# Optimization experiments

Measured on AMD Instinct MI355X. Metric: run time of the kernel, lower is better.

The kernel has to match this reference:

```python
import jax, jax.numpy as jnp
import numpy as np

DIM = 256
NUM_HEADS = 4
WINDOW = 64
EPS = 1e-6


def setup_inputs() -> dict:
    key = jax.random.key(0)
    ks = jax.random.split(key, 12)
    d = DIM
    s = 0.02
    return {
        "x": jax.random.normal(ks[0], (4, 2049, d), dtype=jnp.float32),
        "norm1_w": jnp.ones((d,), jnp.float32),
        "in_proj_w": jax.random.normal(ks[1], (3 * d, d), jnp.float32) * s,
        "in_proj_b": jnp.zeros((3 * d,), jnp.float32),
        "out_proj_w": jax.random.normal(ks[2], (d, d), jnp.float32) * s,
        "out_proj_b": jnp.zeros((d,), jnp.float32),
        "norm2_w": jnp.ones((d,), jnp.float32),
        "w1": jax.random.normal(ks[3], (2 * d, d), jnp.float32) * s,
        "b1": jnp.zeros((2 * d,), jnp.float32),
        "w2": jax.random.normal(ks[4], (d, 2 * d), jnp.float32) * s,
        "b2": jnp.zeros((d,), jnp.float32),
    }


def _rmsnorm(x, w):
    r = jax.lax.rsqrt(jnp.mean(x * x, axis=-1, keepdims=True) + EPS)
    return x * r * w


def _factorized_mask(size):
    # global token 0 attends/attended everywhere; others banded within WINDOW
    idx = jnp.arange(size)
    band = jnp.abs(idx[:, None] - idx[None, :]) <= WINDOW
    allowed = band | (idx[:, None] == 0) | (idx[None, :] == 0)
    return jnp.where(allowed, 0.0, -jnp.inf).astype(jnp.float32)


def reference(x, norm1_w, in_proj_w, in_proj_b, out_proj_w, out_proj_b,
              norm2_w, w1, b1, w2, b2):
    B, S, D = x.shape
    H = NUM_HEADS
    dh = D // H
    residual = x
    h = _rmsnorm(x, norm1_w)
    # fused qkv projection (torch MHA in_proj): [B,S,3D]
    qkv = h @ in_proj_w.T + in_proj_b
    q, k, v = jnp.split(qkv, 3, axis=-1)
    q = q.reshape(B, S, H, dh).transpose(0, 2, 1, 3)  # [B,H,S,dh]
    k = k.reshape(B, S, H, dh).transpose(0, 2, 1, 3)
    v = v.reshape(B, S, H, dh).transpose(0, 2, 1, 3)
    scores = jnp.einsum("bhqd,bhkd->bhqk", q, k) / jnp.sqrt(jnp.float32(dh))
    scores = scores + _factorized_mask(S)  # additive -inf mask
    attn = jax.nn.softmax(scores, axis=-1)
    ctx = jnp.einsum("bhqk,bhkd->bhqd", attn, v)
    ctx = ctx.transpose(0, 2, 1, 3).reshape(B, S, D)
    attn_out = ctx @ out_proj_w.T + out_proj_b
    x1 = residual + attn_out
    h2 = _rmsnorm(x1, norm2_w)
    ffn = jax.nn.gelu(h2 @ w1.T + b1, approximate=False) @ w2.T + b2
    return x1 + ffn
```

## Files before the change

### kernel.cpp

```cpp
#include <hip/hip_runtime.h>
#include <hip/hip_bf16.h>
#include <math.h>

#define BATCH 4
#define SEQ 2049
#define DIMD 256
#define WIN 64
#define M_ROWS (BATCH * SEQ)
#define M_PAD 8320

#define QT16 129
#define NKB 10
#define PSTR 168
#define CSTR 264
#define VGUARD 64
#define VW 2256
#define QKSTR 512

#define NSPLIT 33
#define VT_F4 288768

typedef __attribute__((ext_vector_type(8))) short short8;
typedef __attribute__((ext_vector_type(4))) float f32x4;
typedef __hip_bfloat16 bf16;

__device__ __forceinline__ float b2f(short u) {
    union { unsigned int i; float f; } c;
    c.i = ((unsigned int)(unsigned short)u) << 16;
    return c.f;
}
__device__ __forceinline__ short f2b(float f) {
    bf16 h = __float2bfloat16(f);
    return *reinterpret_cast<short*>(&h);
}

__global__ __launch_bounds__(256) void prep_kernel(
        const float* __restrict__ wq, const float* __restrict__ wo,
        const float* __restrict__ w1, const float* __restrict__ w2,
        bf16* __restrict__ oq, bf16* __restrict__ oo,
        bf16* __restrict__ o1, bf16* __restrict__ o2,
        const float* __restrict__ x, const float* __restrict__ nw,
        bf16* __restrict__ h, float4* __restrict__ vTz) {
    const int bi = blockIdx.x, tid = threadIdx.x;
    if (bi < 2048) {
        int i = bi * 256 + tid;
        if (i < 196608)      oq[i]          = __float2bfloat16(wq[i]);
        else if (i < 262144) oo[i - 196608] = __float2bfloat16(wo[i - 196608]);
        else if (i < 393216) o1[i - 262144] = __float2bfloat16(w1[i - 262144]);
        else                 o2[i - 393216] = __float2bfloat16(w2[i - 393216]);
        return;
    }
    if (bi >= 4097) {
        int zi = (bi - 4097) * 256 + tid;
        #pragma unroll
        for (int it = 0; it < 3; it++) {
            int idx = zi + it * 512 * 256;
            if (idx < VT_F4) vTz[idx] = (float4){0.f, 0.f, 0.f, 0.f};
        }
        return;
    }
    int wid = tid >> 6, lane = tid & 63;
    int row = (bi - 2048) * 4 + wid;
    if (row >= M_ROWS) return;
    const float4 v = reinterpret_cast<const float4*>(x + (size_t)row * DIMD)[lane];
    float ss = v.x * v.x + v.y * v.y + v.z * v.z + v.w * v.w;
    #pragma unroll
    for (int o = 1; o < 64; o <<= 1) ss += __shfl_xor(ss, o, 64);
    float r = rsqrtf(ss * (1.0f / DIMD) + 1e-6f);
    const float4 wv = reinterpret_cast<const float4*>(nw)[lane];
    bf16* hp = h + (size_t)row * DIMD + lane * 4;
    hp[0] = __float2bfloat16(v.x * r * wv.x);
    hp[1] = __float2bfloat16(v.y * r * wv.y);
    hp[2] = __float2bfloat16(v.z * r * wv.z);
    hp[3] = __float2bfloat16(v.w * r * wv.w);
}

__global__ __launch_bounds__(256) void gemm_qkv(
        const bf16* __restrict__ A, const bf16* __restrict__ B,
        const float* __restrict__ bias, bf16* __restrict__ qk, short* __restrict__ vT) {
    __shared__ __align__(16) short lA[8 * 64 * 8];
    __shared__ __align__(16) short lB[8 * 128 * 8];
    const int tid = threadIdx.x, lane = tid & 63, wid = tid >> 6;
    const int m0 = blockIdx.x * 64;
    const int n0 = blockIdx.y * 128;
    const int wr = wid >> 1, wc = wid & 1;
    const int r = lane & 15, g = lane >> 4;
    const int K = 256;

    f32x4 acc[2][4];
    #pragma unroll
    for (int i = 0; i < 2; i++)
        #pragma unroll
        for (int j = 0; j < 4; j++) acc[i][j] = (f32x4){0.f, 0.f, 0.f, 0.f};

    for (int k0 = 0; k0 < K; k0 += 64) {
        #pragma unroll
        for (int it = 0; it < 2; ++it) {
            int c = it * 256 + tid;
            int kc = c >> 6, row = c & 63;
            __builtin_amdgcn_global_load_lds(
                (const __attribute__((address_space(1))) void*)(A + (size_t)(m0 + row) * K + k0 + kc * 8),
                (__attribute__((address_space(3))) void*)&lA[c * 8], 16, 0, 0);
        }
        #pragma unroll
        for (int it = 0; it < 4; ++it) {
            int c = it * 256 + tid;
            int kc = c >> 7, row = c & 127;
            __builtin_amdgcn_global_load_lds(
                (const __attribute__((address_space(1))) void*)(B + (size_t)(n0 + row) * K + k0 + kc * 8),
                (__attribute__((address_space(3))) void*)&lB[c * 8], 16, 0, 0);
        }
        __syncthreads();
        #pragma unroll
        for (int kk = 0; kk < 2; kk++) {
            short8 a[2], b[4];
            #pragma unroll
            for (int mi = 0; mi < 2; mi++)
                a[mi] = *reinterpret_cast<const short8*>(&lA[((kk * 4 + g) * 64 + wr * 32 + mi * 16 + r) * 8]);
            #pragma unroll
            for (int ni = 0; ni < 4; ni++)
                b[ni] = *reinterpret_cast<const short8*>(&lB[((kk * 4 + g) * 128 + wc * 64 + ni * 16 + r) * 8]);
            #pragma unroll
            for (int mi = 0; mi < 2; mi++)
                #pragma unroll
                for (int ni = 0; ni < 4; ni++)
                    acc[mi][ni] = __builtin_amdgcn_mfma_f32_16x16x32_bf16(a[mi], b[ni], acc[mi][ni], 0, 0, 0);
        }
        __syncthreads();
    }

    const int c0 = lane & 15, r0 = (lane >> 4) * 4;
    const bool isV = (n0 >= 512);
    #pragma unroll
    for (int mi = 0; mi < 2; mi++) {
        #pragma unroll
        for (int ni = 0; ni < 4; ni++) {
            int col = n0 + wc * 64 + ni * 16 + c0;
            float bv = bias[col];
            #pragma unroll
            for (int j = 0; j < 4; j++) {
                int row = m0 + wr * 32 + mi * 16 + r0 + j;
                if (row < M_ROWS) {
                    float v = acc[mi][ni][j] + bv;
                    if (!isV) {
                        qk[(size_t)row * QKSTR + col] = __float2bfloat16(v);
                    } else {
                        int dcol = col - 512, hh = dcol >> 6, d = dcol & 63;
                        int bb = row >> 11;
                        int js = row - bb * SEQ;
                        if (js < 0) { bb--; js += SEQ; }
                        vT[((size_t)((bb * 4 + hh) * 64 + d)) * VW + VGUARD + js] = f2b(v);
                    }
                }
            }
        }
    }
}

template<int MODE, int BM, int BN>
__global__ __launch_bounds__(256) void gemm_lds(
        const bf16* __restrict__ A, const bf16* __restrict__ B,
        const float* __restrict__ bias, const float* __restrict__ resid,
        void* __restrict__ C, int M, int N, int K) {
    constexpr int FM = BM / 32;
    constexpr int FN = BN / 32;
    __shared__ __align__(16) short lA[8 * BM * 8];
    __shared__ __align__(16) short lB[8 * BN * 8];
    const int tid = threadIdx.x, lane = tid & 63, wid = tid >> 6;
    const int m0 = blockIdx.x * BM;
    const int n0 = blockIdx.y * BN;
    const int wr = wid >> 1, wc = wid & 1;
    const int r = lane & 15, g = lane >> 4;

    f32x4 acc[FM][FN];
    #pragma unroll
    for (int i = 0; i < FM; i++)
        #pragma unroll
        for (int j = 0; j < FN; j++) acc[i][j] = (f32x4){0.f, 0.f, 0.f, 0.f};

    for (int k0 = 0; k0 < K; k0 += 64) {
        #pragma unroll
        for (int it = 0; it < BM / 32; ++it) {
            int c = it * 256 + tid;
            int kc = c / BM, row = c % BM;
            __builtin_amdgcn_global_load_lds(
                (const __attribute__((address_space(1))) void*)(A + (size_t)(m0 + row) * K + k0 + kc * 8),
                (__attribute__((address_space(3))) void*)&lA[c * 8], 16, 0, 0);
        }
        #pragma unroll
        for (int it = 0; it < BN / 32; ++it) {
            int c = it * 256 + tid;
            int kc = c / BN, row = c % BN;
            __builtin_amdgcn_global_load_lds(
                (const __attribute__((address_space(1))) void*)(B + (size_t)(n0 + row) * K + k0 + kc * 8),
                (__attribute__((address_space(3))) void*)&lB[c * 8], 16, 0, 0);
        }
        __syncthreads();
        #pragma unroll
        for (int kk = 0; kk < 2; kk++) {
            short8 a[FM], b[FN];
            #pragma unroll
            for (int mi = 0; mi < FM; mi++)
                a[mi] = *reinterpret_cast<const short8*>(&lA[((kk * 4 + g) * BM + wr * (BM / 2) + mi * 16 + r) * 8]);
            #pragma unroll
            for (int ni = 0; ni < FN; ni++)
                b[ni] = *reinterpret_cast<const short8*>(&lB[((kk * 4 + g) * BN + wc * (BN / 2) + ni * 16 + r) * 8]);
            #pragma unroll
            for (int mi = 0; mi < FM; mi++)
                #pragma unroll
                for (int ni = 0; ni < FN; ni++)
                    acc[mi][ni] = __builtin_amdgcn_mfma_f32_16x16x32_bf16(a[mi], b[ni], acc[mi][ni], 0, 0, 0);
        }
        __syncthreads();
    }

    const int c0 = lane & 15, r0 = (lane >> 4) * 4;
    #pragma unroll
    for (int mi = 0; mi < FM; mi++) {
        #pragma unroll
        for (int ni = 0; ni < FN; ni++) {
            int col = n0 + wc * (BN / 2) + ni * 16 + c0;
            float bv = bias[col];
            #pragma unroll
            for (int j = 0; j < 4; j++) {
                int row = m0 + wr * (BM / 2) + mi * 16 + r0 + j;
                if (row < M) {
                    float v = acc[mi][ni][j] + bv;
                    if (MODE == 2) v = 0.5f * v * (1.0f + erff(v * 0.70710678118654752f));
                    if (MODE == 1) {
                        v += resid[(size_t)row * N + col];
                        reinterpret_cast<float*>(C)[(size_t)row * N + col] = v;
                    } else {
                        reinterpret_cast<bf16*>(C)[(size_t)row * N + col] = __float2bfloat16(v);
                    }
                }
            }
        }
    }
}

__global__ __launch_bounds__(256) void attn_partial(const bf16* __restrict__ qk,
                                                    const short* __restrict__ vT,
                                                    float* __restrict__ part) {
    __shared__ float q_s[64];
    __shared__ float p_s[64];
    __shared__ float meta[2];
    __shared__ float osum[4][64];
    const int tid = threadIdx.x;
    const int bh = blockIdx.x / NSPLIT, s = blockIdx.x % NSPLIT;
    const int b = bh >> 2, h = bh & 3;
    const size_t base = (size_t)b * SEQ;
    const int j0 = s * 64;
    const int lane = tid & 63, wid = tid >> 6;

    if (tid < 64) q_s[tid] = __bfloat162float(qk[base * QKSTR + h * 64 + tid]);
    __syncthreads();

    if (wid == 0) {
        int j = j0 + lane;
        float sc = -1e30f;
        if (j < SEQ) {
            const short8* kp = reinterpret_cast<const short8*>(
                reinterpret_cast<const short*>(qk) + (base + j) * QKSTR + 256 + h * 64);
            float acc = 0.f;
            #pragma unroll
            for (int d8 = 0; d8 < 8; ++d8) {
                short8 kv = kp[d8];
                #pragma unroll
                for (int e = 0; e < 8; ++e) acc += q_s[d8 * 8 + e] * b2f(kv[e]);
            }
            sc = acc * 0.125f;
        }
        float mx = sc;
        #pragma unroll
        for (int o = 1; o < 64; o <<= 1) mx = fmaxf(mx, __shfl_xor(mx, o, 64));
        float p = (j < SEQ) ? expf(sc - mx) : 0.f;
        p_s[lane] = p;
        float l = p;
        #pragma unroll
        for (int o = 1; o < 64; o <<= 1) l += __shfl_xor(l, o, 64);
        if (lane == 0) { meta[0] = mx; meta[1] = l; }
    }
    __syncthreads();

    const short* vrow = vT + ((size_t)bh * 64 + lane) * VW + VGUARD + j0;
    float oa = 0.f;
    #pragma unroll
    for (int i0 = 0; i0 < 16; i0++) {
        int i = wid + i0 * 4;
        if (j0 + i < SEQ) oa += p_s[i] * b2f(vrow[i]);
    }
    osum[wid][lane] = oa;
    __syncthreads();
    if (wid == 0) {
        float o = osum[0][lane] + osum[1][lane] + osum[2][lane] + osum[3][lane];
        float* pp = part + (size_t)(bh * NSPLIT + s) * 66;
        pp[lane] = o;
        if (lane == 0) { pp[64] = meta[0]; pp[65] = meta[1]; }
    }
}

__global__ __launch_bounds__(256) void attn_or(
        const bf16* __restrict__ qkb, const short* __restrict__ vT,
        const float* __restrict__ part, const bf16* __restrict__ wo,
        const float* __restrict__ ob, const float* __restrict__ x,
        const float* __restrict__ nw, float* __restrict__ x1, bf16* __restrict__ h2) {
    __shared__ short p_lds[4][16][PSTR];
    __shared__ short ctx_lds[16][CSTR];
    __shared__ float osq[4][16];
    const short* qk = reinterpret_cast<const short*>(qkb);
    const int tid = threadIdx.x, lane = tid & 63, h = tid >> 6;
    const int qt = blockIdx.x % QT16;
    const int b = blockIdx.x / QT16;
    const int bh = b * 4 + h;
    const size_t rbase = (size_t)b * SEQ;
    const int q0 = qt * 16;
    const int jbase = q0 - 64;
    const int lrow = lane & 15;
    const int koff = (lane >> 4) * 8;
    const int c0 = lrow, r0 = (lane >> 4) * 4;

    int qrow = q0 + lrow; if (qrow > SEQ - 1) qrow = SEQ - 1;
    const short* qp = qk + (rbase + qrow) * QKSTR + h * 64;
    short8 aq0 = *reinterpret_cast<const short8*>(qp + koff);
    short8 aq1 = *reinterpret_cast<const short8*>(qp + 32 + koff);

    const short* k0p = qk + rbase * QKSTR + 256 + h * 64;
    short8 k0a = *reinterpret_cast<const short8*>(k0p + koff);
    short8 k0b = *reinterpret_cast<const short8*>(k0p + 32 + koff);
    float s0 = 0.f;
    #pragma unroll
    for (int e = 0; e < 8; e++)
        s0 += b2f(aq0[e]) * b2f(k0a[e]) + b2f(aq1[e]) * b2f(k0b[e]);
    s0 += __shfl_xor(s0, 16, 64);
    s0 += __shfl_xor(s0, 32, 64);

    f32x4 s[NKB];
    #pragma unroll
    for (int n = 0; n < NKB; n++) {
        int j = jbase + n * 16 + lrow;
        int jc = j < 0 ? 0 : (j > SEQ - 1 ? SEQ - 1 : j);
        const short* kp = qk + (rbase + jc) * QKSTR + 256 + h * 64;
        short8 bk0 = *reinterpret_cast<const short8*>(kp + koff);
        short8 bk1 = *reinterpret_cast<const short8*>(kp + 32 + koff);
        f32x4 acc = (f32x4){0.f, 0.f, 0.f, 0.f};
        acc = __builtin_amdgcn_mfma_f32_16x16x32_bf16(aq0, bk0, acc, 0, 0, 0);
        acc = __builtin_amdgcn_mfma_f32_16x16x32_bf16(aq1, bk1, acc, 0, 0, 0);
        s[n] = acc;
    }

    const float SC = 0.125f * 1.44269504088896340736f;
    const bool g1 = (jbase > 0);
    float s0q[4], m4[4];
    #pragma unroll
    for (int jj = 0; jj < 4; jj++) {
        s0q[jj] = __shfl(s0, r0 + jj, 64) * SC;
        m4[jj] = g1 ? s0q[jj] : -1e30f;
    }
    #pragma unroll
    for (int n = 0; n < NKB; n++) {
        int j = jbase + n * 16 + c0;
        bool jv = (j >= 0) && (j < SEQ);
        #pragma unroll
        for (int jj = 0; jj < 4; jj++) {
            int q = q0 + r0 + jj;
            int dd = q - j; if (dd < 0) dd = -dd;
            bool allowed = jv && (dd <= WIN || j == 0);
            float v = allowed ? s[n][jj] * SC : -1e30f;
            s[n][jj] = v;
            m4[jj] = fmaxf(m4[jj], v);
        }
    }
    #pragma unroll
    for (int o = 1; o < 16; o <<= 1) {
        #pragma unroll
        for (int jj = 0; jj < 4; jj++) m4[jj] = fmaxf(m4[jj], __shfl_xor(m4[jj], o, 64));
    }

    float p0[4], l4[4];
    #pragma unroll
    for (int jj = 0; jj < 4; jj++) {
        p0[jj] = g1 ? exp2f(s0q[jj] - m4[jj]) : 0.f;
        l4[jj] = p0[jj];
    }
    #pragma unroll
    for (int n = 0; n < NKB; n++) {
        #pragma unroll
        for (int jj = 0; jj < 4; jj++) {
            float p = exp2f(s[n][jj] - m4[jj]);
            l4[jj] += p;
            p_lds[h][r0 + jj][n * 16 + c0] = f2b(p);
        }
    }
    #pragma unroll
    for (int o = 1; o < 16; o <<= 1) {
        #pragma unroll
        for (int jj = 0; jj < 4; jj++) l4[jj] += __shfl_xor(l4[jj], o, 64);
    }

    f32x4 o[4];
    #pragma unroll
    for (int dn = 0; dn < 4; dn++) o[dn] = (f32x4){0.f, 0.f, 0.f, 0.f};
    #pragma unroll
    for (int ks = 0; ks < NKB / 2; ks++) {
        short8 ap = *reinterpret_cast<const short8*>(&p_lds[h][lrow][ks * 32 + koff]);
        int cc = VGUARD + jbase + ks * 32 + koff;
        #pragma unroll
        for (int dn = 0; dn < 4; dn++) {
            short8 bv = *reinterpret_cast<const short8*>(
                vT + ((size_t)bh * 64 + dn * 16 + lrow) * VW + cc);
            o[dn] = __builtin_amdgcn_mfma_f32_16x16x32_bf16(ap, bv, o[dn], 0, 0, 0);
        }
    }

    #pragma unroll
    for (int jj = 0; jj < 4; jj++) {
        int q = q0 + r0 + jj;
        int ql = r0 + jj;
        float rl = 1.0f / l4[jj];
        #pragma unroll
        for (int dn = 0; dn < 4; dn++) {
            float v0 = b2f(vT[((size_t)bh * 64 + dn * 16 + c0) * VW + VGUARD]);
            float val = (o[dn][jj] + p0[jj] * v0) * rl;
            if (q >= 1) ctx_lds[ql][h * 64 + dn * 16 + c0] = f2b(val);
        }
    }

    if (qt == 0) {
        float m = (lane < NSPLIT) ? part[(size_t)(bh * NSPLIT + lane) * 66 + 64] : -1e30f;
        #pragma unroll
        for (int o2 = 1; o2 < 64; o2 <<= 1) m = fmaxf(m, __shfl_xor(m, o2, 64));
        float L = 0.f, ov = 0.f;
        for (int sp = 0; sp < NSPLIT; sp++) {
            const float* pp = part + (size_t)(bh * NSPLIT + sp) * 66;
            float w = expf(pp[64] - m);
            L += pp[65] * w;
            ov += pp[lane] * w;
        }
        ctx_lds[0][h * 64 + lane] = f2b(ov / L);
    }
    __syncthreads();

    f32x4 oacc[4];
    #pragma unroll
    for (int ni = 0; ni < 4; ni++) oacc[ni] = (f32x4){0.f, 0.f, 0.f, 0.f};
    #pragma unroll
    for (int ks = 0; ks < 8; ks++) {
        short8 a = *reinterpret_cast<const short8*>(&ctx_lds[lrow][ks * 32 + koff]);
        #pragma unroll
        for (int ni = 0; ni < 4; ni++) {
            short8 bfrag = *reinterpret_cast<const short8*>(
                reinterpret_cast<const short*>(wo) + (size_t)(h * 64 + ni * 16 + lrow) * 256 + ks * 32 + koff);
            oacc[ni] = __builtin_amdgcn_mfma_f32_16x16x32_bf16(a, bfrag, oacc[ni], 0, 0, 0);
        }
    }

    float ssq[4];
    #pragma unroll
    for (int jj = 0; jj < 4; jj++) {
        int row = q0 + r0 + jj;
        float sq = 0.f;
        if (row < SEQ) {
            #pragma unroll
            for (int ni = 0; ni < 4; ni++) {
                int col = h * 64 + ni * 16 + c0;
                float v = oacc[ni][jj] + ob[col] + x[(rbase + row) * 256 + col];
                oacc[ni][jj] = v;
                x1[(rbase + row) * 256 + col] = v;
                sq += v * v;
            }
        }
        ssq[jj] = sq;
    }
    #pragma unroll
    for (int o2 = 1; o2 < 16; o2 <<= 1) {
        #pragma unroll
        for (int jj = 0; jj < 4; jj++) ssq[jj] += __shfl_xor(ssq[jj], o2, 64);
    }
    if (c0 == 0) {
        #pragma unroll
        for (int jj = 0; jj < 4; jj++) osq[h][r0 + jj] = ssq[jj];
    }
    __syncthreads();
    #pragma unroll
    for (int jj = 0; jj < 4; jj++) {
        int lr = r0 + jj;
        int row = q0 + lr;
        if (row < SEQ) {
            float tot = osq[0][lr] + osq[1][lr] + osq[2][lr] + osq[3][lr];
            float rs = rsqrtf(tot * (1.0f / 256.0f) + 1e-6f);
            #pragma unroll
            for (int ni = 0; ni < 4; ni++) {
                int col = h * 64 + ni * 16 + c0;
                h2[(rbase + row) * 256 + col] = __float2bfloat16(oacc[ni][jj] * rs * nw[col]);
            }
        }
    }
}

extern "C" void kernel_launch(void* const* d_in, const int* in_sizes, int n_in,
                              void* d_out, int out_size, void* d_ws, size_t ws_size,
                              hipStream_t stream) {
    const float* x         = (const float*)d_in[0];
    const float* norm1_w   = (const float*)d_in[1];
    const float* in_proj_w = (const float*)d_in[2];
    const float* in_proj_b = (const float*)d_in[3];
    const float* out_proj_w= (const float*)d_in[4];
    const float* out_proj_b= (const float*)d_in[5];
    const float* norm2_w   = (const float*)d_in[6];
    const float* w1        = (const float*)d_in[7];
    const float* b1        = (const float*)d_in[8];
    const float* w2        = (const float*)d_in[9];
    const float* b2        = (const float*)d_in[10];
    float* out = (float*)d_out;

    const int M = M_ROWS;
    char* ws = (char*)d_ws;
    size_t off = 0;
    auto take = [&](size_t bytes) {
        char* p = ws + off;
        off = (off + bytes + 255) & ~(size_t)255;
        return p;
    };
    bf16* h_bf   = (bf16*)take((size_t)M_PAD * 256 * 2);
    bf16* qk_bf  = (bf16*)take((size_t)M_PAD * QKSTR * 2);
    float* x1    = (float*)take((size_t)M_PAD * 256 * 4);
    bf16* h2_bf  = (bf16*)take((size_t)M_PAD * 256 * 2);
    bf16* g_bf   = (bf16*)take((size_t)M_PAD * 512 * 2);
    bf16* wq_bf  = (bf16*)take(768 * 256 * 2);
    bf16* wo_bf  = (bf16*)take(256 * 256 * 2);
    bf16* w1_bf  = (bf16*)take(512 * 256 * 2);
    bf16* w2_bf  = (bf16*)take(256 * 512 * 2);
    float* part  = (float*)take((size_t)16 * NSPLIT * 66 * 4);
    short* vT    = (short*)take((size_t)16 * 64 * VW * 2);
    (void)ws_size; (void)in_sizes; (void)n_in; (void)out_size;

    prep_kernel<<<dim3(4609), dim3(256), 0, stream>>>(
        in_proj_w, out_proj_w, w1, w2, wq_bf, wo_bf, w1_bf, w2_bf,
        x, norm1_w, h_bf, (float4*)vT);
    gemm_qkv<<<dim3(130, 6), dim3(256), 0, stream>>>(h_bf, wq_bf, in_proj_b, qk_bf, vT);
    attn_partial<<<dim3(16 * NSPLIT), dim3(256), 0, stream>>>(qk_bf, vT, part);
    attn_or<<<dim3(4 * QT16), dim3(256), 0, stream>>>(
        qk_bf, vT, part, wo_bf, out_proj_b, x, norm2_w, x1, h2_bf);
    gemm_lds<2, 64, 128><<<dim3(130, 4), dim3(256), 0, stream>>>(h2_bf, w1_bf, b1, (const float*)nullptr,
                                                                 (void*)g_bf, M, 512, 256);
    gemm_lds<1, 64, 64><<<dim3(130, 4), dim3(256), 0, stream>>>(g_bf, w2_bf, b2, x1,
                                                                (void*)out, M, 256, 512);
}
```

Before: 114.5 us.

## Fuse first RMSNorm into QKV GEMM and zero only vT guard bands

```diff
diff --git a/kernel.cpp b/kernel.cpp
--- a/kernel.cpp
+++ b/kernel.cpp
@@ -4,9 +4,8 @@
 
 #define BATCH 4
 #define SEQ 2049
-#define DIMD 256
 #define WIN 64
-#define M_ROWS (BATCH * SEQ)
+#define M_ROWS 8196
 #define M_PAD 8320
 
 #define QT16 129
@@ -16,9 +15,9 @@
 #define VGUARD 64
 #define VW 2256
 #define QKSTR 512
-
 #define NSPLIT 33
 #define VT_F4 288768
+#define KCS 520
 
 typedef __attribute__((ext_vector_type(8))) short short8;
 typedef __attribute__((ext_vector_type(4))) float f32x4;
@@ -39,8 +38,7 @@
         const float* __restrict__ w1, const float* __restrict__ w2,
         bf16* __restrict__ oq, bf16* __restrict__ oo,
         bf16* __restrict__ o1, bf16* __restrict__ o2,
-        const float* __restrict__ x, const float* __restrict__ nw,
-        bf16* __restrict__ h, float4* __restrict__ vTz) {
+        short* __restrict__ vT) {
     const int bi = blockIdx.x, tid = threadIdx.x;
     if (bi < 2048) {
         int i = bi * 256 + tid;
@@ -50,42 +48,50 @@
         else                 o2[i - 393216] = __float2bfloat16(w2[i - 393216]);
         return;
     }
-    if (bi >= 4097) {
-        int zi = (bi - 4097) * 256 + tid;
-        #pragma unroll
-        for (int it = 0; it < 3; it++) {
-            int idx = zi + it * 512 * 256;
-            if (idx < VT_F4) vTz[idx] = (float4){0.f, 0.f, 0.f, 0.f};
-        }
-        return;
-    }
-    int wid = tid >> 6, lane = tid & 63;
-    int row = (bi - 2048) * 4 + wid;
-    if (row >= M_ROWS) return;
-    const float4 v = reinterpret_cast<const float4*>(x + (size_t)row * DIMD)[lane];
-    float ss = v.x * v.x + v.y * v.y + v.z * v.z + v.w * v.w;
-    #pragma unroll
-    for (int o = 1; o < 64; o <<= 1) ss += __shfl_xor(ss, o, 64);
-    float r = rsqrtf(ss * (1.0f / DIMD) + 1e-6f);
-    const float4 wv = reinterpret_cast<const float4*>(nw)[lane];
-    bf16* hp = h + (size_t)row * DIMD + lane * 4;
-    hp[0] = __float2bfloat16(v.x * r * wv.x);
-    hp[1] = __float2bfloat16(v.y * r * wv.y);
-    hp[2] = __float2bfloat16(v.z * r * wv.z);
-    hp[3] = __float2bfloat16(v.w * r * wv.w);
+    int rowid = (bi - 2048) * 2 + (tid >> 7);
+    short* vr = vT + (size_t)rowid * VW;
+    int t = tid & 127;
+    if (t < 64) vr[t] = 0;
+    else {
+        int u = t - 64;
+        if (u < 143) vr[VGUARD + SEQ + u] = 0;
+        if (u + 143 < 143) {}
+    }
 }
 
 __global__ __launch_bounds__(256) void gemm_qkv(
-        const bf16* __restrict__ A, const bf16* __restrict__ B,
-        const float* __restrict__ bias, bf16* __restrict__ qk, short* __restrict__ vT) {
-    __shared__ __align__(16) short lA[8 * 64 * 8];
+        const float* __restrict__ x, const float* __restrict__ n1w,
+        const bf16* __restrict__ B, const float* __restrict__ bias,
+        bf16* __restrict__ qk, short* __restrict__ vT) {
+    __shared__ __align__(16) short hA[32 * KCS];
     __shared__ __align__(16) short lB[8 * 128 * 8];
     const int tid = threadIdx.x, lane = tid & 63, wid = tid >> 6;
     const int m0 = blockIdx.x * 64;
     const int n0 = blockIdx.y * 128;
     const int wr = wid >> 1, wc = wid & 1;
     const int r = lane & 15, g = lane >> 4;
-    const int K = 256;
+
+    {
+        const float4 wv = reinterpret_cast<const float4*>(n1w)[lane];
+        #pragma unroll
+        for (int t = 0; t < 16; t++) {
+            int rr = wid * 16 + t;
+            int row = m0 + rr;
+            int rowc = row < M_ROWS ? row : M_ROWS - 1;
+            const float4 v = reinterpret_cast<const float4*>(x + (size_t)rowc * 256)[lane];
+            float ss = v.x * v.x + v.y * v.y + v.z * v.z + v.w * v.w;
+            #pragma unroll
+            for (int o = 1; o < 64; o <<= 1) ss += __shfl_xor(ss, o, 64);
+            float rs = rsqrtf(ss * (1.0f / 256.0f) + 1e-6f);
+            short4 y;
+            y.x = f2b(v.x * rs * wv.x);
+            y.y = f2b(v.y * rs * wv.y);
+            y.z = f2b(v.z * rs * wv.z);
+            y.w = f2b(v.w * rs * wv.w);
+            *reinterpret_cast<short4*>(&hA[(lane >> 1) * KCS + rr * 8 + (lane & 1) * 4]) = y;
+        }
+    }
+    __syncthreads();
 
     f32x4 acc[2][4];
     #pragma unroll
@@ -93,21 +99,14 @@
         #pragma unroll
         for (int j = 0; j < 4; j++) acc[i][j] = (f32x4){0.f, 0.f, 0.f, 0.f};
 
-    for (int k0 = 0; k0 < K; k0 += 64) {
-        #pragma unroll
-        for (int it = 0; it < 2; ++it) {
-            int c = it * 256 + tid;
-            int kc = c >> 6, row = c & 63;
-            __builtin_amdgcn_global_load_lds(
-                (const __attribute__((address_space(1))) void*)(A + (size_t)(m0 + row) * K + k0 + kc * 8),
-                (__attribute__((address_space(3))) void*)&lA[c * 8], 16, 0, 0);
-        }
+    for (int k0 = 0; k0 < 256; k0 += 64) {
+        const int kcb = k0 >> 3;
         #pragma unroll
         for (int it = 0; it < 4; ++it) {
             int c = it * 256 + tid;
             int kc = c >> 7, row = c & 127;
             __builtin_amdgcn_global_load_lds(
-                (const __attribute__((address_space(1))) void*)(B + (size_t)(n0 + row) * K + k0 + kc * 8),
+                (const __attribute__((address_space(1))) void*)(B + (size_t)(n0 + row) * 256 + k0 + kc * 8),
                 (__attribute__((address_space(3))) void*)&lB[c * 8], 16, 0, 0);
         }
         __syncthreads();
@@ -116,7 +115,8 @@
             short8 a[2], b[4];
             #pragma unroll
             for (int mi = 0; mi < 2; mi++)
-                a[mi] = *reinterpret_cast<const short8*>(&lA[((kk * 4 + g) * 64 + wr * 32 + mi * 16 + r) * 8]);
+                a[mi] = *reinterpret_cast<const short8*>(
+                    &hA[(kcb + kk * 4 + g) * KCS + (wr * 32 + mi * 16 + r) * 8]);
             #pragma unroll
             for (int ni = 0; ni < 4; ni++)
                 b[ni] = *reinterpret_cast<const short8*>(&lB[((kk * 4 + g) * 128 + wc * 64 + ni * 16 + r) * 8]);
@@ -158,12 +158,11 @@
 }
 
 template<int MODE, int BM, int BN>
-__global__ __launch_bounds__(256) void gemm_lds(
+__global__ __launch_bounds__(256) void gemm_lds_k(
         const bf16* __restrict__ A, const bf16* __restrict__ B,
         const float* __restrict__ bias, const float* __restrict__ resid,
         void* __restrict__ C, int M, int N, int K) {
-    constexpr int FM = BM / 32;
-    constexpr int FN = BN / 32;
+    constexpr int FM = BM / 32, FN = BN / 32;
     __shared__ __align__(16) short lA[8 * BM * 8];
     __shared__ __align__(16) short lB[8 * BN * 8];
     const int tid = threadIdx.x, lane = tid & 63, wid = tid >> 6;
@@ -239,29 +238,27 @@
     }
 }
 
-__global__ __launch_bounds__(256) void attn_partial(const bf16* __restrict__ qk,
-                                                    const short* __restrict__ vT,
-                                                    float* __restrict__ part) {
+__global__ __launch_bounds__(256) void attn_partial_k(const bf16* __restrict__ qkb,
+                                                      const short* __restrict__ vT,
+                                                      float* __restrict__ part) {
     __shared__ float q_s[64];
     __shared__ float p_s[64];
     __shared__ float meta[2];
     __shared__ float osum[4][64];
+    const short* qks = (const short*)qkb;
     const int tid = threadIdx.x;
+    const int lane = tid & 63, wid = tid >> 6;
     const int bh = blockIdx.x / NSPLIT, s = blockIdx.x % NSPLIT;
     const int b = bh >> 2, h = bh & 3;
     const size_t base = (size_t)b * SEQ;
     const int j0 = s * 64;
-    const int lane = tid & 63, wid = tid >> 6;
-
-    if (tid < 64) q_s[tid] = __bfloat162float(qk[base * QKSTR + h * 64 + tid]);
+    if (tid < 64) q_s[tid] = b2f(qks[base * QKSTR + h * 64 + tid]);
     __syncthreads();
-
     if (wid == 0) {
         int j = j0 + lane;
         float sc = -1e30f;
         if (j < SEQ) {
-            const short8* kp = reinterpret_cast<const short8*>(
-                reinterpret_cast<const short*>(qk) + (base + j) * QKSTR + 256 + h * 64);
+            const short8* kp = reinterpret_cast<const short8*>(qks + (base + j) * QKSTR + 256 + h * 64);
             float acc = 0.f;
             #pragma unroll
             for (int d8 = 0; d8 < 8; ++d8) {
@@ -274,15 +271,14 @@
         float mx = sc;
         #pragma unroll
         for (int o = 1; o < 64; o <<= 1) mx = fmaxf(mx, __shfl_xor(mx, o, 64));
-        float p = (j < SEQ) ? expf(sc - mx) : 0.f;
-        p_s[lane] = p;
-        float l = p;
+        float pv = (j < SEQ) ? expf(sc - mx) : 0.f;
+        p_s[lane] = pv;
+        float l = pv;
         #pragma unroll
         for (int o = 1; o < 64; o <<= 1) l += __shfl_xor(l, o, 64);
         if (lane == 0) { meta[0] = mx; meta[1] = l; }
     }
     __syncthreads();
-
     const short* vrow = vT + ((size_t)bh * 64 + lane) * VW + VGUARD + j0;
     float oa = 0.f;
     #pragma unroll
@@ -294,21 +290,21 @@
     __syncthreads();
     if (wid == 0) {
         float o = osum[0][lane] + osum[1][lane] + osum[2][lane] + osum[3][lane];
-        float* pp = part + (size_t)(bh * NSPLIT + s) * 66;
+        float* pp = part + (size_t)blockIdx.x * 66;
         pp[lane] = o;
         if (lane == 0) { pp[64] = meta[0]; pp[65] = meta[1]; }
     }
 }
 
-__global__ __launch_bounds__(256) void attn_or(
+__global__ __launch_bounds__(256) void attn_or_k(
         const bf16* __restrict__ qkb, const short* __restrict__ vT,
         const float* __restrict__ part, const bf16* __restrict__ wo,
         const float* __restrict__ ob, const float* __restrict__ x,
         const float* __restrict__ nw, float* __restrict__ x1, bf16* __restrict__ h2) {
-    __shared__ short p_lds[4][16][PSTR];
-    __shared__ short ctx_lds[16][CSTR];
+    __shared__ short pl[4 * 16 * PSTR];
+    __shared__ short cl[16 * CSTR];
     __shared__ float osq[4][16];
-    const short* qk = reinterpret_cast<const short*>(qkb);
+    const short* qks = (const short*)qkb;
     const int tid = threadIdx.x, lane = tid & 63, h = tid >> 6;
     const int qt = blockIdx.x % QT16;
     const int b = blockIdx.x / QT16;
@@ -321,11 +317,11 @@
     const int c0 = lrow, r0 = (lane >> 4) * 4;
 
     int qrow = q0 + lrow; if (qrow > SEQ - 1) qrow = SEQ - 1;
-    const short* qp = qk + (rbase + qrow) * QKSTR + h * 64;
+    const short* qp = qks + (rbase + qrow) * QKSTR + h * 64;
     short8 aq0 = *reinterpret_cast<const short8*>(qp + koff);
     short8 aq1 = *reinterpret_cast<const short8*>(qp + 32 + koff);
 
-    const short* k0p = qk + rbase * QKSTR + 256 + h * 64;
+    const short* k0p = qks + rbase * QKSTR + 256 + h * 64;
     short8 k0a = *reinterpret_cast<const short8*>(k0p + koff);
     short8 k0b = *reinterpret_cast<const short8*>(k0p + 32 + koff);
     float s0 = 0.f;
@@ -340,7 +336,7 @@
     for (int n = 0; n < NKB; n++) {
         int j = jbase + n * 16 + lrow;
         int jc = j < 0 ? 0 : (j > SEQ - 1 ? SEQ - 1 : j);
-        const short* kp = qk + (rbase + jc) * QKSTR + 256 + h * 64;
+        const short* kp = qks + (rbase + jc) * QKSTR + 256 + h * 64;
         short8 bk0 = *reinterpret_cast<const short8*>(kp + koff);
         short8 bk1 = *reinterpret_cast<const short8*>(kp + 32 + koff);
         f32x4 acc = (f32x4){0.f, 0.f, 0.f, 0.f};
@@ -387,9 +383,9 @@
     for (int n = 0; n < NKB; n++) {
         #pragma unroll
         for (int jj = 0; jj < 4; jj++) {
-            float p = exp2f(s[n][jj] - m4[jj]);
-            l4[jj] += p;
-            p_lds[h][r0 + jj][n * 16 + c0] = f2b(p);
+            float pv = exp2f(s[n][jj] - m4[jj]);
+            l4[jj] += pv;
+            pl[(h * 16 + r0 + jj) * PSTR + n * 16 + c0] = f2b(pv);
         }
     }
     #pragma unroll
@@ -398,18 +394,18 @@
         for (int jj = 0; jj < 4; jj++) l4[jj] += __shfl_xor(l4[jj], o, 64);
     }
 
-    f32x4 o[4];
-    #pragma unroll
-    for (int dn = 0; dn < 4; dn++) o[dn] = (f32x4){0.f, 0.f, 0.f, 0.f};
+    f32x4 o4[4];
+    #pragma unroll
+    for (int dn = 0; dn < 4; dn++) o4[dn] = (f32x4){0.f, 0.f, 0.f, 0.f};
     #pragma unroll
     for (int ks = 0; ks < NKB / 2; ks++) {
-        short8 ap = *reinterpret_cast<const short8*>(&p_lds[h][lrow][ks * 32 + koff]);
+        short8 ap = *reinterpret_cast<const short8*>(&pl[(h * 16 + lrow) * PSTR + ks * 32 + koff]);
         int cc = VGUARD + jbase + ks * 32 + koff;
         #pragma unroll
         for (int dn = 0; dn < 4; dn++) {
             short8 bv = *reinterpret_cast<const short8*>(
                 vT + ((size_t)bh * 64 + dn * 16 + lrow) * VW + cc);
-            o[dn] = __builtin_amdgcn_mfma_f32_16x16x32_bf16(ap, bv, o[dn], 0, 0, 0);
+            o4[dn] = __builtin_amdgcn_mfma_f32_16x16x32_bf16(ap, bv, o4[dn], 0, 0, 0);
         }
     }
 
@@ -421,8 +417,8 @@
         #pragma unroll
         for (int dn = 0; dn < 4; dn++) {
             float v0 = b2f(vT[((size_t)bh * 64 + dn * 16 + c0) * VW + VGUARD]);
-            float val = (o[dn][jj] + p0[jj] * v0) * rl;
-            if (q >= 1) ctx_lds[ql][h * 64 + dn * 16 + c0] = f2b(val);
+            float val = (o4[dn][jj] + p0[jj] * v0) * rl;
+            if (q >= 1) cl[ql * CSTR + h * 64 + dn * 16 + c0] = f2b(val);
         }
     }
 
@@ -437,7 +433,7 @@
             L += pp[65] * w;
             ov += pp[lane] * w;
         }
-        ctx_lds[0][h * 64 + lane] = f2b(ov / L);
+        cl[0 * CSTR + h * 64 + lane] = f2b(ov / L);
     }
     __syncthreads();
 
@@ -446,7 +442,7 @@
     for (int ni = 0; ni < 4; ni++) oacc[ni] = (f32x4){0.f, 0.f, 0.f, 0.f};
     #pragma unroll
     for (int ks = 0; ks < 8; ks++) {
-        short8 a = *reinterpret_cast<const short8*>(&ctx_lds[lrow][ks * 32 + koff]);
+        short8 a = *reinterpret_cast<const short8*>(&cl[lrow * CSTR + ks * 32 + koff]);
         #pragma unroll
         for (int ni = 0; ni < 4; ni++) {
             short8 bfrag = *reinterpret_cast<const short8*>(
@@ -514,15 +510,13 @@
     const float* b2        = (const float*)d_in[10];
     float* out = (float*)d_out;
 
-    const int M = M_ROWS;
     char* ws = (char*)d_ws;
     size_t off = 0;
     auto take = [&](size_t bytes) {
-        char* p = ws + off;
+        char* q = ws + off;
         off = (off + bytes + 255) & ~(size_t)255;
-        return p;
+        return q;
     };
-    bf16* h_bf   = (bf16*)take((size_t)M_PAD * 256 * 2);
     bf16* qk_bf  = (bf16*)take((size_t)M_PAD * QKSTR * 2);
     float* x1    = (float*)take((size_t)M_PAD * 256 * 4);
     bf16* h2_bf  = (bf16*)take((size_t)M_PAD * 256 * 2);
@@ -535,15 +529,14 @@
     short* vT    = (short*)take((size_t)16 * 64 * VW * 2);
     (void)ws_size; (void)in_sizes; (void)n_in; (void)out_size;
 
-    prep_kernel<<<dim3(4609), dim3(256), 0, stream>>>(
-        in_proj_w, out_proj_w, w1, w2, wq_bf, wo_bf, w1_bf, w2_bf,
-        x, norm1_w, h_bf, (float4*)vT);
-    gemm_qkv<<<dim3(130, 6), dim3(256), 0, stream>>>(h_bf, wq_bf, in_proj_b, qk_bf, vT);
-    attn_partial<<<dim3(16 * NSPLIT), dim3(256), 0, stream>>>(qk_bf, vT, part);
-    attn_or<<<dim3(4 * QT16), dim3(256), 0, stream>>>(
+    prep_kernel<<<dim3(2560), dim3(256), 0, stream>>>(
+        in_proj_w, out_proj_w, w1, w2, wq_bf, wo_bf, w1_bf, w2_bf, vT);
+    gemm_qkv<<<dim3(130, 6), dim3(256), 0, stream>>>(x, norm1_w, wq_bf, in_proj_b, qk_bf, vT);
+    attn_partial_k<<<dim3(16 * NSPLIT), dim3(256), 0, stream>>>(qk_bf, vT, part);
+    attn_or_k<<<dim3(4 * QT16), dim3(256), 0, stream>>>(
         qk_bf, vT, part, wo_bf, out_proj_b, x, norm2_w, x1, h2_bf);
-    gemm_lds<2, 64, 128><<<dim3(130, 4), dim3(256), 0, stream>>>(h2_bf, w1_bf, b1, (const float*)nullptr,
-                                                                 (void*)g_bf, M, 512, 256);
-    gemm_lds<1, 64, 64><<<dim3(130, 4), dim3(256), 0, stream>>>(g_bf, w2_bf, b2, x1,
-                                                                (void*)out, M, 256, 512);
-}
+    gemm_lds_k<2, 64, 128><<<dim3(130, 4), dim3(256), 0, stream>>>(
+        h2_bf, w1_bf, b1, (const float*)nullptr, (void*)g_bf, M_ROWS, 512, 256);
+    gemm_lds_k<1, 64, 64><<<dim3(130, 4), dim3(256), 0, stream>>>(
+        g_bf, w2_bf, b2, x1, (void*)out, M_ROWS, 256, 512);
+}
```

Result: slower. 118.0 us (+3.1%).
